# Performance work log

Hardware: AMD Instinct MI355X
Metric: run time of the kernel (lower is better)

The kernel has to match this reference:

```python
import math
import jax, jax.numpy as jnp
import numpy as np


def _bilinear_maps_sample(kv_feats, shapes_wh, start_ids, locs, map_ids):
    """Bilinear sampling from concatenated multi-level 2D maps.

    kv_feats: [BH, S, C] flattened (row-major, per level) feature maps
    shapes_wh: [L, 2] int (W, H) per level
    start_ids: [L] int start offset of each level in S
    locs: [BH, M, 2] normalized (x, y) in [0, 1]
    map_ids: [BH, M] int level index per sample
    returns [BH, M, C]
    """
    wh = shapes_wh[map_ids]                      # [BH, M, 2]
    W = wh[..., 0]
    H = wh[..., 1]
    start = start_ids[map_ids]                   # [BH, M]
    Wf = W.astype(locs.dtype)
    Hf = H.astype(locs.dtype)
    x = locs[..., 0] * Wf - 0.5                  # align_corners=False convention
    y = locs[..., 1] * Hf - 0.5
    x0 = jnp.floor(x)
    y0 = jnp.floor(y)
    out = jnp.zeros(locs.shape[:-1] + (kv_feats.shape[-1],), kv_feats.dtype)
    for dx in (0, 1):
        for dy in (0, 1):
            xi = x0 + dx
            yi = y0 + dy
            w = (1.0 - jnp.abs(x - xi)) * (1.0 - jnp.abs(y - yi))
            valid = (xi >= 0) & (xi < Wf) & (yi >= 0) & (yi < Hf)
            xi_c = jnp.clip(xi, 0, Wf - 1).astype(jnp.int32)
            yi_c = jnp.clip(yi, 0, Hf - 1).astype(jnp.int32)
            idx = start + yi_c * W + xi_c        # [BH, M]
            f = jnp.take_along_axis(kv_feats, idx[..., None], axis=1)
            out = out + jnp.where(valid, w, 0.0)[..., None] * f
    return out


def setup_inputs() -> dict:
    key = jax.random.key(0)
    ks = jax.random.split(key, 10)
    B, N, L, Hh, P = 2, 2048, 5, 8, 4
    in_size, sample_size = 256, 256
    qk_size, value_size = 256, 256
    kv_size = qk_size + value_size

    shapes = np.array([[128, 128], [64, 64], [32, 32], [16, 16], [8, 8]], np.int32)  # (H, W)
    flat = (shapes[:, 0] * shapes[:, 1]).astype(np.int64)
    start = np.concatenate([[0], np.cumsum(flat)[:-1]]).astype(np.int32)
    S = int(flat.sum())  # 21824

    # sampling_offsets bias: canonical Deformable-DETR grid init
    thetas = np.arange(Hh, dtype=np.float32) * (2.0 * math.pi / Hh)
    grid = np.stack([np.cos(thetas), np.sin(thetas)], axis=1)
    grid = grid / np.abs(grid).max(axis=1, keepdims=True)
    grid = np.tile(grid.reshape(Hh, 1, 1, 2), (1, L, 1, 1))
    sizes = np.arange(1, P + 1, dtype=np.float32).reshape(1, 1, P, 1)
    b_off = (sizes * grid).reshape(-1)           # [H*L*P*2]

    def lin(k, out_d, in_d):
        return jax.random.normal(k, (out_d, in_d), jnp.float32) * (1.0 / math.sqrt(in_d))

    return {
        "in_feats": jax.random.normal(ks[0], (B, N, in_size), jnp.float32),
        "sample_priors": jax.random.uniform(ks[1], (B, N, L, 2), jnp.float32),
        "sample_feats": jax.random.normal(ks[2], (B, S, sample_size), jnp.float32),
        "sample_map_shapes": jnp.asarray(shapes),
        "sample_map_start_ids": jnp.asarray(start),
        "W_off": jax.random.normal(ks[3], (Hh * L * P * 2, in_size), jnp.float32) * 0.02,
        "b_off": jnp.asarray(b_off),
        "W_q": lin(ks[4], qk_size, in_size),
        "b_q": jnp.zeros((qk_size,), jnp.float32),
        "W_kv": lin(ks[5], kv_size, sample_size),
        "b_kv": jnp.zeros((kv_size,), jnp.float32),
        "point_encs": jax.random.normal(ks[6], (Hh, L * P, qk_size // Hh), jnp.float32) * 0.02,
        "W_out": lin(ks[7], in_size, value_size),
        "b_out": jnp.zeros((in_size,), jnp.float32),
    }


def reference(in_feats, sample_priors, sample_feats, sample_map_shapes,
              sample_map_start_ids, W_off, b_off, W_q, b_q, W_kv, b_kv,
              point_encs, W_out, b_out):
    B, N = in_feats.shape[:2]
    Hh, LP, dqk = point_encs.shape
    L = sample_map_shapes.shape[0]
    P = LP // L

    # sampling offsets + locations (priors last dim == 2 path)
    off = (in_feats @ W_off.T + b_off).reshape(B, N, Hh, L, P, 2)
    shapes_wh = sample_map_shapes[:, ::-1]                      # fliplr -> (W, H)
    norm = shapes_wh.astype(in_feats.dtype)[None, None, None, :, None, :]
    locs = sample_priors[:, :, None, :, None, :] + off / norm    # [B,N,H,L,P,2]

    q = (in_feats @ W_q.T + b_q).reshape(B, N, Hh, dqk)
    kv = sample_feats @ W_kv.T + b_kv                            # [B,S,kv_size]
    ck = kv.shape[-1] // Hh
    kv = kv.reshape(B, -1, Hh, ck).transpose(0, 2, 1, 3).reshape(B * Hh, -1, ck)

    locs = locs.transpose(0, 2, 1, 3, 4, 5).reshape(B * Hh, N * L * P, 2)
    map_ids = jnp.broadcast_to(jnp.arange(L, dtype=jnp.int32)[None, None, :, None],
                               (B * Hh, N, L, P)).reshape(B * Hh, -1)

    sampled = _bilinear_maps_sample(kv, shapes_wh, sample_map_start_ids, locs, map_ids)
    sampled = sampled.reshape(B, Hh, N, LP, ck).transpose(0, 2, 1, 3, 4)  # [B,N,H,LP,ck]

    keys = sampled[..., :dqk] + point_encs                       # [B,N,H,LP,dqk]
    vals = sampled[..., dqk:]                                    # [B,N,H,LP,cv]
    attn = jax.nn.softmax(
        jnp.einsum('bnhd,bnhpd->bnhp', q / math.sqrt(dqk), keys), axis=-1)
    weighted = jnp.einsum('bnhp,bnhpd->bnhd', attn, vals).reshape(B, N, -1)
    return weighted @ W_out.T + b_out
```

## Files before the change

### kernel.cpp

```cpp
#include <hip/hip_runtime.h>
#include <cstddef>

#define B_  2
#define N_  2048
#define L_  5
#define HH  8
#define P_  4
#define S_  21824
#define DQK 32

using bf16x8 = __attribute__((ext_vector_type(8))) short;
using f32x4  = __attribute__((ext_vector_type(4))) float;
using us8    = __attribute__((ext_vector_type(8))) unsigned short;

__device__ __forceinline__ unsigned short f2b(float f) {
  unsigned u = __builtin_bit_cast(unsigned, f);
  u += 0x7FFFu + ((u >> 16) & 1u);
  return (unsigned short)(u >> 16);
}
__device__ __forceinline__ float b2f(unsigned short h) {
  return __builtin_bit_cast(float, ((unsigned)h) << 16);
}

__device__ __forceinline__ void gld_lds16(const void* g, void* l) {
  __builtin_amdgcn_global_load_lds(
      (const __attribute__((address_space(1))) unsigned int*)g,
      (__attribute__((address_space(3))) unsigned int*)l, 16, 0, 0);
}

template <int CTRL>
__device__ __forceinline__ float dppadd(float v) {
  const int x = __builtin_bit_cast(int, v);
  return v + __builtin_bit_cast(float,
      __builtin_amdgcn_update_dpp(x, x, CTRL, 0xF, 0xF, false));
}

#define E0 1396736
#define E1 1527808
#define E2 1658880
#define E3 1675264
#define E4 1683456
#define E5 1691648
#define E6 1703936
#define E7 1716224

__device__ __forceinline__ void cvt8_plain(const float* s, unsigned short* d, int u) {
  const float4 a = ((const float4*)s)[2 * u];
  const float4 b = ((const float4*)s)[2 * u + 1];
  us8 o;
  o[0] = f2b(a.x); o[1] = f2b(a.y); o[2] = f2b(a.z); o[3] = f2b(a.w);
  o[4] = f2b(b.x); o[5] = f2b(b.y); o[6] = f2b(b.z); o[7] = f2b(b.w);
  ((us8*)d)[u] = o;
}
__device__ __forceinline__ unsigned short f2b_lo(float x) {
  return f2b(x - b2f(f2b(x)));
}
__device__ __forceinline__ void cvt8_lo(const float* s, unsigned short* d, int u) {
  const float4 a = ((const float4*)s)[2 * u];
  const float4 b = ((const float4*)s)[2 * u + 1];
  us8 o;
  o[0] = f2b_lo(a.x); o[1] = f2b_lo(a.y); o[2] = f2b_lo(a.z); o[3] = f2b_lo(a.w);
  o[4] = f2b_lo(b.x); o[5] = f2b_lo(b.y); o[6] = f2b_lo(b.z); o[7] = f2b_lo(b.w);
  ((us8*)d)[u] = o;
}

__global__ __launch_bounds__(256) void cvt_all(
    const float* __restrict__ sfeats, const float* __restrict__ in_feats,
    const float* __restrict__ W_kv, const float* __restrict__ W_q,
    const float* __restrict__ W_out, const float* __restrict__ W_off,
    unsigned short* __restrict__ sf_bf, unsigned short* __restrict__ if_hi,
    unsigned short* __restrict__ if_lo, unsigned short* __restrict__ wkv_bf,
    unsigned short* __restrict__ wq_bf, unsigned short* __restrict__ wout_bf,
    unsigned short* __restrict__ woff_hi, unsigned short* __restrict__ woff_lo) {
  const int i = blockIdx.x * 256 + threadIdx.x;
  if      (i < E0) cvt8_plain(sfeats, sf_bf, i);
  else if (i < E1) cvt8_plain(in_feats, if_hi, i - E0);
  else if (i < E2) cvt8_lo(in_feats, if_lo, i - E1);
  else if (i < E3) cvt8_plain(W_kv, wkv_bf, i - E2);
  else if (i < E4) cvt8_plain(W_q, wq_bf, i - E3);
  else if (i < E5) cvt8_plain(W_out, wout_bf, i - E4);
  else if (i < E6) {
    const int u = i - E5;
    if ((u >> 5) < 320) cvt8_plain(W_off, woff_hi, u);
    else ((us8*)woff_hi)[u] = (us8)0;
  } else {
    const int u = i - E6;
    if ((u >> 5) < 320) cvt8_lo(W_off, woff_lo, u);
    else ((us8*)woff_lo)[u] = (us8)0;
  }
}

__device__ __forceinline__ void mfma_tile_k256(
    const unsigned short* __restrict__ Ap, const unsigned short* __restrict__ Wp,
    unsigned short* As, unsigned short* Bs,
    int row0, int col0, int wv, int wr, int wc, int fr, int fq,
    int srow, int sch, f32x4 (&acc)[4][4]) {
  for (int k0 = 0; k0 < 256; k0 += 64) {
#pragma unroll
    for (int i = 0; i < 4; ++i) {
      const int r = i * 32 + srow;
      const int ca = sch ^ (r & 7);
      gld_lds16(Ap + (size_t)(row0 + r) * 256 + k0 + ca * 8,
                As + (size_t)(i * 32 + wv * 8) * 64);
      gld_lds16(Wp + (size_t)(col0 + r) * 256 + k0 + ca * 8,
                Bs + (size_t)(i * 32 + wv * 8) * 64);
    }
    __syncthreads();
#pragma unroll
    for (int kk = 0; kk < 2; ++kk) {
      bf16x8 af[4], bfv[4];
#pragma unroll
      for (int i = 0; i < 4; ++i) {
        const int ar = wr * 64 + i * 16 + fr;
        const int cha = (kk * 4 + fq) ^ (ar & 7);
        af[i] = *(const bf16x8*)(As + ar * 64 + cha * 8);
        const int br = wc * 64 + i * 16 + fr;
        const int chb = (kk * 4 + fq) ^ (br & 7);
        bfv[i] = *(const bf16x8*)(Bs + br * 64 + chb * 8);
      }
#pragma unroll
      for (int i = 0; i < 4; ++i)
#pragma unroll
        for (int j = 0; j < 4; ++j)
          acc[i][j] = __builtin_amdgcn_mfma_f32_16x16x32_bf16(
              af[i], bfv[j], acc[i][j], 0, 0, 0);
    }
    __syncthreads();
  }
}

__global__ __launch_bounds__(256) void ubergemm(
    const unsigned short* __restrict__ sf_bf,
    const unsigned short* __restrict__ wkv_bf,
    const unsigned short* __restrict__ if_hi,
    const unsigned short* __restrict__ if_lo,
    const unsigned short* __restrict__ woff_hi,
    const unsigned short* __restrict__ woff_lo,
    const unsigned short* __restrict__ wq_bf,
    const float* __restrict__ b_kv, const float* __restrict__ b_off,
    const float* __restrict__ b_q,
    unsigned short* __restrict__ kvt, float* __restrict__ offb,
    float* __restrict__ qb) {
  __shared__ __align__(16) unsigned short As[128 * 64];
  __shared__ __align__(16) unsigned short Bs[128 * 64];

  const int tid = threadIdx.x;
  const int lane = tid & 63;
  const int wv = tid >> 6;
  const int wr = wv >> 1, wc = wv & 1;
  const int fr = lane & 15, fq = lane >> 4;
  const int srow = tid >> 3;
  const int sch = tid & 7;
  const int bx = blockIdx.x;

  int mode, nseg, row0, col0, ldc = 0, nbias = 0;
  const unsigned short *A0, *W0, *A1 = nullptr, *W1 = nullptr,
                       *A2 = nullptr, *W2 = nullptr;
  const float* bias;
  float* Cf = nullptr;
  if (bx < 1364) {
    mode = 1; nseg = 1; A0 = sf_bf; W0 = wkv_bf; bias = b_kv;
    col0 = (bx & 3) * 128; row0 = (bx >> 2) * 128;
  } else if (bx < 1460) {
    const int t = bx - 1364;
    mode = 0; nseg = 3;
    A0 = if_hi; W0 = woff_hi; A1 = if_hi; W1 = woff_lo; A2 = if_lo; W2 = woff_hi;
    bias = b_off; Cf = offb; ldc = 384; nbias = 320;
    col0 = (t % 3) * 128; row0 = (t / 3) * 128;
  } else {
    const int t = bx - 1460;
    mode = 0; nseg = 1; A0 = if_hi; W0 = wq_bf; bias = b_q;
    Cf = qb; ldc = 256; nbias = 256;
    col0 = (t & 1) * 128; row0 = (t >> 1) * 128;
  }

  f32x4 acc[4][4] = {};
  for (int s = 0; s < nseg; ++s) {
    const unsigned short* Ap = (s == 0) ? A0 : (s == 1) ? A1 : A2;
    const unsigned short* Wp = (s == 0) ? W0 : (s == 1) ? W1 : W2;
    mfma_tile_k256(Ap, Wp, As, Bs, row0, col0, wv, wr, wc, fr, fq, srow, sch, acc);
  }

#pragma unroll
  for (int j = 0; j < 4; ++j) {
    const int n = col0 + wc * 64 + j * 16 + fr;
    const float bv = (mode == 1) ? bias[n] : ((n < nbias) ? bias[n] : 0.f);
#pragma unroll
    for (int i = 0; i < 4; ++i) {
      const int mbase = row0 + wr * 64 + i * 16 + fq * 4;
#pragma unroll
      for (int r = 0; r < 4; ++r) {
        const int m = mbase + r;
        if (mode == 1) {
          const int b = (m >= S_) ? 1 : 0;
          const int s = m - b * S_;
          const int h = n >> 6, c = n & 63;
          kvt[((size_t)(b * HH + h) * S_ + s) * 64 + c] = f2b(acc[i][j][r] + bv);
        } else {
          Cf[(size_t)m * ldc + n] = acc[i][j][r] + bv;
        }
      }
    }
  }
}

__global__ __launch_bounds__(256) void gemm_out(
    const unsigned short* __restrict__ A, const unsigned short* __restrict__ Wt,
    const float* __restrict__ bias, float* __restrict__ C) {
  __shared__ __align__(16) unsigned short As[128 * 64];
  __shared__ __align__(16) unsigned short Bs[128 * 64];
  const int tid = threadIdx.x;
  const int lane = tid & 63;
  const int wv = tid >> 6;
  const int wr = wv >> 1, wc = wv & 1;
  const int fr = lane & 15, fq = lane >> 4;
  const int row0 = blockIdx.y * 128, col0 = blockIdx.x * 128;
  const int srow = tid >> 3, sch = tid & 7;
  f32x4 acc[4][4] = {};
  mfma_tile_k256(A, Wt, As, Bs, row0, col0, wv, wr, wc, fr, fq, srow, sch, acc);
#pragma unroll
  for (int j = 0; j < 4; ++j) {
    const int n = col0 + wc * 64 + j * 16 + fr;
    const float bv = bias[n];
#pragma unroll
    for (int i = 0; i < 4; ++i) {
      const int mbase = row0 + wr * 64 + i * 16 + fq * 4;
#pragma unroll
      for (int r = 0; r < 4; ++r)
        C[(size_t)(mbase + r) * 256 + n] = acc[i][j][r] + bv;
    }
  }
}

__global__ __launch_bounds__(256) void sample_attn4(
    const unsigned short* __restrict__ kvt,
    const float* __restrict__ offb,
    const float* __restrict__ qb,
    const float* __restrict__ priors,
    const int* __restrict__ shapes,
    const int* __restrict__ starts,
    const float* __restrict__ pencs,
    unsigned short* __restrict__ wtd) {
  __shared__ __align__(16) int pbuf[4][20][8];
  const int wv = threadIdx.x >> 6;
  const int lane = threadIdx.x & 63;
  const int beta = blockIdx.x;
  const int sig = (beta & 7) * 2 + ((beta >> 3) & 1);
  const int chunk = beta >> 4;
  const int h = sig & 7;
  const int b = sig >> 3;
  const int bn = b * N_ + chunk * 4 + wv;
  const int j = lane & 31;
  const int half = lane >> 5;

  if (lane < 20) {
    const int pp = lane;
    const int l = pp >> 2;
    const float2 oxy = *(const float2*)(offb + (size_t)bn * 384 + h * 40 + pp * 2);
    const float2 pxy = *(const float2*)(priors + ((size_t)bn * 5 + l) * 2);
    const int Wd = shapes[l * 2 + 1];
    const int Hd = shapes[l * 2 + 0];
    const int st = starts[l];
    const float Wf = (float)Wd, Hf = (float)Hd;
    const float x = (pxy.x + oxy.x / Wf) * Wf - 0.5f;
    const float y = (pxy.y + oxy.y / Hf) * Hf - 0.5f;
    const float x0f = floorf(x), y0f = floorf(y);
    const float fx = x - x0f, fy = y - y0f;
    const int xi = (int)x0f, yi = (int)y0f;
    int a[4]; float w[4];
#pragma unroll
    for (int dy = 0; dy < 2; ++dy)
#pragma unroll
      for (int dx = 0; dx < 2; ++dx) {
        const int xc = xi + dx, yc = yi + dy;
        const bool valid = (xc >= 0) & (xc < Wd) & (yc >= 0) & (yc < Hd);
        const float wt = (dx ? fx : 1.f - fx) * (dy ? fy : 1.f - fy);
        const int xcc = min(max(xc, 0), Wd - 1);
        const int ycc = min(max(yc, 0), Hd - 1);
        a[dy * 2 + dx] = (st + ycc * Wd + xcc) * 32;
        w[dy * 2 + dx] = valid ? wt : 0.f;
      }
    *(int4*)&pbuf[wv][pp][0] = make_int4(a[0], a[1], a[2], a[3]);
    *(float4*)&pbuf[wv][pp][4] = make_float4(w[0], w[1], w[2], w[3]);
  }

  const int jc = j & 15;
  float2 q2 = *(const float2*)(qb + (size_t)bn * 256 + h * DQK + 2 * jc);
  q2.x *= 0.17677669529663687f;
  q2.y *= 0.17677669529663687f;
  float qpe[10];
#pragma unroll
  for (int i = 0; i < 10; ++i) {
    const float2 pe = *(const float2*)(
        pencs + ((size_t)h * 20 + 2 * i + half) * DQK + 2 * jc);
    qpe[i] = q2.x * pe.x + q2.y * pe.y;
  }

  const unsigned* kvd = (const unsigned*)(kvt + (size_t)(b * HH + h) * (S_ * 64));
  int4 aa[2]; float4 ww[2]; unsigned g[2][4];
  aa[0] = *(const int4*)&pbuf[wv][half][0];
  ww[0] = *(const float4*)&pbuf[wv][half][4];
  g[0][0] = kvd[(unsigned)aa[0].x + j];
  g[0][1] = kvd[(unsigned)aa[0].y + j];
  g[0][2] = kvd[(unsigned)aa[0].z + j];
  g[0][3] = kvd[(unsigned)aa[0].w + j];

  float2 sam[10];
  float lg[10];
#pragma unroll
  for (int i = 0; i < 10; ++i) {
    const int cur = i & 1, nxt = cur ^ 1;
    if (i < 9) {
      aa[nxt] = *(const int4*)&pbuf[wv][2 * (i + 1) + half][0];
      ww[nxt] = *(const float4*)&pbuf[wv][2 * (i + 1) + half][4];
      g[nxt][0] = kvd[(unsigned)aa[nxt].x + j];
      g[nxt][1] = kvd[(unsigned)aa[nxt].y + j];
      g[nxt][2] = kvd[(unsigned)aa[nxt].z + j];
      g[nxt][3] = kvd[(unsigned)aa[nxt].w + j];
    }
    const float4 wt = ww[cur];
    const unsigned g0 = g[cur][0], g1 = g[cur][1], g2 = g[cur][2], g3 = g[cur][3];
    const float lo0 = __builtin_bit_cast(float, g0 << 16);
    const float hi0 = __builtin_bit_cast(float, g0 & 0xFFFF0000u);
    const float lo1 = __builtin_bit_cast(float, g1 << 16);
    const float hi1 = __builtin_bit_cast(float, g1 & 0xFFFF0000u);
    const float lo2 = __builtin_bit_cast(float, g2 << 16);
    const float hi2 = __builtin_bit_cast(float, g2 & 0xFFFF0000u);
    const float lo3 = __builtin_bit_cast(float, g3 << 16);
    const float hi3 = __builtin_bit_cast(float, g3 & 0xFFFF0000u);
    float vx = wt.x * lo0;  vx = fmaf(wt.y, lo1, vx);
    vx = fmaf(wt.z, lo2, vx); vx = fmaf(wt.w, lo3, vx);
    float vy = wt.x * hi0;  vy = fmaf(wt.y, hi1, vy);
    vy = fmaf(wt.z, hi2, vy); vy = fmaf(wt.w, hi3, vy);
    sam[i].x = vx; sam[i].y = vy;
    float part = (j < 16) ? fmaf(q2.x, vx, fmaf(q2.y, vy, qpe[i])) : 0.f;
    part = dppadd<0xB1>(part);
    part = dppadd<0x4E>(part);
    part = dppadd<0x124>(part);
    part = dppadd<0x128>(part);
    lg[i] = part + __shfl_xor(part, 16, 64);
  }

  float mx = lg[0];
#pragma unroll
  for (int i = 1; i < 10; ++i) mx = fmaxf(mx, lg[i]);
  mx = fmaxf(mx, __shfl_xor(mx, 32, 64));
  float se = 0.f;
#pragma unroll
  for (int i = 0; i < 10; ++i) {
    lg[i] = __expf(lg[i] - mx);
    se += lg[i];
  }
  se += __shfl_xor(se, 32, 64);
  const float inv = 1.f / se;

  float ax = 0.f, ay = 0.f;
#pragma unroll
  for (int i = 0; i < 10; ++i) {
    ax = fmaf(lg[i], sam[i].x, ax);
    ay = fmaf(lg[i], sam[i].y, ay);
  }
  ax += __shfl_xor(ax, 32, 64);
  ay += __shfl_xor(ay, 32, 64);

  if (half == 0 && j >= 16) {
    const unsigned u = (unsigned)f2b(ax * inv) | ((unsigned)f2b(ay * inv) << 16);
    ((unsigned*)wtd)[(size_t)bn * 128 + h * 16 + (j - 16)] = u;
  }
}

extern "C" void kernel_launch(void* const* d_in, const int* in_sizes, int n_in,
                              void* d_out, int out_size, void* d_ws, size_t ws_size,
                              hipStream_t stream) {
  const float* in_feats = (const float*)d_in[0];
  const float* priors   = (const float*)d_in[1];
  const float* sfeats   = (const float*)d_in[2];
  const int*   shapes   = (const int*)d_in[3];
  const int*   starts   = (const int*)d_in[4];
  const float* W_off    = (const float*)d_in[5];
  const float* b_off    = (const float*)d_in[6];
  const float* W_q      = (const float*)d_in[7];
  const float* b_q      = (const float*)d_in[8];
  const float* W_kv     = (const float*)d_in[9];
  const float* b_kv     = (const float*)d_in[10];
  const float* pencs    = (const float*)d_in[11];
  const float* W_out    = (const float*)d_in[12];
  const float* b_out    = (const float*)d_in[13];
  float* out = (float*)d_out;

  char* w = (char*)d_ws;
  unsigned short* kvt = (unsigned short*)w;
  w += (size_t)B_ * HH * S_ * 64 * 2;
  unsigned short* sf_bf = (unsigned short*)w;
  w += (size_t)B_ * S_ * 256 * 2;
  unsigned short* if_hi = (unsigned short*)w; w += (size_t)4096 * 256 * 2;
  unsigned short* if_lo = (unsigned short*)w; w += (size_t)4096 * 256 * 2;
  unsigned short* wkv_bf = (unsigned short*)w;  w += (size_t)512 * 256 * 2;
  unsigned short* wq_bf  = (unsigned short*)w;  w += (size_t)256 * 256 * 2;
  unsigned short* wout_bf = (unsigned short*)w; w += (size_t)256 * 256 * 2;
  unsigned short* woff_hi = (unsigned short*)w; w += (size_t)384 * 256 * 2;
  unsigned short* woff_lo = (unsigned short*)w; w += (size_t)384 * 256 * 2;
  float* offb = (float*)w;  w += (size_t)4096 * 384 * 4;
  float* qb   = (float*)w;  w += (size_t)4096 * 256 * 4;
  unsigned short* wtd_bf = (unsigned short*)w; w += (size_t)4096 * 256 * 2;

  cvt_all<<<E7 / 256, 256, 0, stream>>>(
      sfeats, in_feats, W_kv, W_q, W_out, W_off,
      sf_bf, if_hi, if_lo, wkv_bf, wq_bf, wout_bf, woff_hi, woff_lo);

  ubergemm<<<1524, 256, 0, stream>>>(
      sf_bf, wkv_bf, if_hi, if_lo, woff_hi, woff_lo, wq_bf,
      b_kv, b_off, b_q, kvt, offb, qb);

  sample_attn4<<<(B_ * N_ * HH) / 4, 256, 0, stream>>>(
      kvt, offb, qb, priors, shapes, starts, pencs, wtd_bf);

  gemm_out<<<dim3(2, 32), 256, 0, stream>>>(wtd_bf, wout_bf, b_out, out);
}
```

Baseline: 99.91 us.

## Fuse sample_feats bf16 conversion into KV GEMM A-tile load

The KV projection GEMM now reads fp32 sample features directly, converting them to bf16 with packed-convert instructions while staging into LDS. This removes the separate conversion pass, which wrote and then re-read a bf16 copy of the largest input. The small offset/query GEMM blocks are moved to the front, and KV tiles are reordered in groups of 8 rows per column for L2 reuse of the A rows. The in_feats hi/lo split is also merged into one pass. The A-tile load is no longer an asynchronous global-to-LDS copy, so it now goes through registers.

```diff
diff --git a/kernel.cpp b/kernel.cpp
--- a/kernel.cpp
+++ b/kernel.cpp
@@ -21,6 +21,11 @@
 __device__ __forceinline__ float b2f(unsigned short h) {
   return __builtin_bit_cast(float, ((unsigned)h) << 16);
 }
+__device__ __forceinline__ unsigned cvtpk(float lo, float hi) {
+  unsigned r;
+  asm("v_cvt_pk_bf16_f32 %0, %1, %2" : "=v"(r) : "v"(lo), "v"(hi));
+  return r;
+}
 
 __device__ __forceinline__ void gld_lds16(const void* g, void* l) {
   __builtin_amdgcn_global_load_lds(
@@ -35,14 +40,12 @@
       __builtin_amdgcn_update_dpp(x, x, CTRL, 0xF, 0xF, false));
 }
 
-#define E0 1396736
-#define E1 1527808
-#define E2 1658880
-#define E3 1675264
-#define E4 1683456
-#define E5 1691648
-#define E6 1703936
-#define E7 1716224
+#define F0 131072
+#define F1 147456
+#define F2 155648
+#define F3 163840
+#define F4 176128
+#define F5 188416
 
 __device__ __forceinline__ void cvt8_plain(const float* s, unsigned short* d, int u) {
   const float4 a = ((const float4*)s)[2 * u];
@@ -63,34 +66,71 @@
   o[4] = f2b_lo(b.x); o[5] = f2b_lo(b.y); o[6] = f2b_lo(b.z); o[7] = f2b_lo(b.w);
   ((us8*)d)[u] = o;
 }
+__device__ __forceinline__ void cvt8_both(const float* s, unsigned short* dh,
+                                          unsigned short* dl, int u) {
+  const float4 a = ((const float4*)s)[2 * u];
+  const float4 b = ((const float4*)s)[2 * u + 1];
+  us8 oh, ol;
+  const float v[8] = {a.x, a.y, a.z, a.w, b.x, b.y, b.z, b.w};
+#pragma unroll
+  for (int k = 0; k < 8; ++k) {
+    const unsigned short h = f2b(v[k]);
+    oh[k] = h;
+    ol[k] = f2b(v[k] - b2f(h));
+  }
+  ((us8*)dh)[u] = oh;
+  ((us8*)dl)[u] = ol;
+}
 
 __global__ __launch_bounds__(256) void cvt_all(
-    const float* __restrict__ sfeats, const float* __restrict__ in_feats,
-    const float* __restrict__ W_kv, const float* __restrict__ W_q,
-    const float* __restrict__ W_out, const float* __restrict__ W_off,
-    unsigned short* __restrict__ sf_bf, unsigned short* __restrict__ if_hi,
-    unsigned short* __restrict__ if_lo, unsigned short* __restrict__ wkv_bf,
-    unsigned short* __restrict__ wq_bf, unsigned short* __restrict__ wout_bf,
-    unsigned short* __restrict__ woff_hi, unsigned short* __restrict__ woff_lo) {
+    const float* __restrict__ in_feats, const float* __restrict__ W_kv,
+    const float* __restrict__ W_q, const float* __restrict__ W_out,
+    const float* __restrict__ W_off,
+    unsigned short* __restrict__ if_hi, unsigned short* __restrict__ if_lo,
+    unsigned short* __restrict__ wkv_bf, unsigned short* __restrict__ wq_bf,
+    unsigned short* __restrict__ wout_bf, unsigned short* __restrict__ woff_hi,
+    unsigned short* __restrict__ woff_lo) {
   const int i = blockIdx.x * 256 + threadIdx.x;
-  if      (i < E0) cvt8_plain(sfeats, sf_bf, i);
-  else if (i < E1) cvt8_plain(in_feats, if_hi, i - E0);
-  else if (i < E2) cvt8_lo(in_feats, if_lo, i - E1);
-  else if (i < E3) cvt8_plain(W_kv, wkv_bf, i - E2);
-  else if (i < E4) cvt8_plain(W_q, wq_bf, i - E3);
-  else if (i < E5) cvt8_plain(W_out, wout_bf, i - E4);
-  else if (i < E6) {
-    const int u = i - E5;
+  if      (i < F0) cvt8_both(in_feats, if_hi, if_lo, i);
+  else if (i < F1) cvt8_plain(W_kv, wkv_bf, i - F0);
+  else if (i < F2) cvt8_plain(W_q, wq_bf, i - F1);
+  else if (i < F3) cvt8_plain(W_out, wout_bf, i - F2);
+  else if (i < F4) {
+    const int u = i - F3;
     if ((u >> 5) < 320) cvt8_plain(W_off, woff_hi, u);
     else ((us8*)woff_hi)[u] = (us8)0;
   } else {
-    const int u = i - E6;
+    const int u = i - F4;
     if ((u >> 5) < 320) cvt8_lo(W_off, woff_lo, u);
     else ((us8*)woff_lo)[u] = (us8)0;
   }
 }
 
-__device__ __forceinline__ void mfma_tile_k256(
+__device__ __forceinline__ void mfma_compute(
+    const unsigned short* As, const unsigned short* Bs,
+    int wr, int wc, int fr, int fq, f32x4 (&acc)[4][4]) {
+#pragma unroll
+  for (int kk = 0; kk < 2; ++kk) {
+    bf16x8 af[4], bfv[4];
+#pragma unroll
+    for (int i = 0; i < 4; ++i) {
+      const int ar = wr * 64 + i * 16 + fr;
+      const int cha = (kk * 4 + fq) ^ (ar & 7);
+      af[i] = *(const bf16x8*)(As + ar * 64 + cha * 8);
+      const int br = wc * 64 + i * 16 + fr;
+      const int chb = (kk * 4 + fq) ^ (br & 7);
+      bfv[i] = *(const bf16x8*)(Bs + br * 64 + chb * 8);
+    }
+#pragma unroll
+    for (int i = 0; i < 4; ++i)
+#pragma unroll
+      for (int j = 0; j < 4; ++j)
+        acc[i][j] = __builtin_amdgcn_mfma_f32_16x16x32_bf16(
+            af[i], bfv[j], acc[i][j], 0, 0, 0);
+  }
+}
+
+__device__ __forceinline__ void mfma_tile_bf16(
     const unsigned short* __restrict__ Ap, const unsigned short* __restrict__ Wp,
     unsigned short* As, unsigned short* Bs,
     int row0, int col0, int wv, int wr, int wc, int fr, int fq,
@@ -106,31 +146,47 @@
                 Bs + (size_t)(i * 32 + wv * 8) * 64);
     }
     __syncthreads();
-#pragma unroll
-    for (int kk = 0; kk < 2; ++kk) {
-      bf16x8 af[4], bfv[4];
-#pragma unroll
-      for (int i = 0; i < 4; ++i) {
-        const int ar = wr * 64 + i * 16 + fr;
-        const int cha = (kk * 4 + fq) ^ (ar & 7);
-        af[i] = *(const bf16x8*)(As + ar * 64 + cha * 8);
-        const int br = wc * 64 + i * 16 + fr;
-        const int chb = (kk * 4 + fq) ^ (br & 7);
-        bfv[i] = *(const bf16x8*)(Bs + br * 64 + chb * 8);
-      }
-#pragma unroll
-      for (int i = 0; i < 4; ++i)
-#pragma unroll
-        for (int j = 0; j < 4; ++j)
-          acc[i][j] = __builtin_amdgcn_mfma_f32_16x16x32_bf16(
-              af[i], bfv[j], acc[i][j], 0, 0, 0);
-    }
+    mfma_compute(As, Bs, wr, wc, fr, fq, acc);
     __syncthreads();
   }
 }
 
+__device__ __forceinline__ void mfma_tile_f32A(
+    const float* __restrict__ Af, const unsigned short* __restrict__ Wp,
+    unsigned short* As, unsigned short* Bs,
+    int row0, int col0, int wv, int wr, int wc, int fr, int fq,
+    int srow, int sch, int tid, f32x4 (&acc)[4][4]) {
+  const int arow = tid >> 1;
+  const int cb = (tid & 1) * 4;
+  for (int k0 = 0; k0 < 256; k0 += 64) {
+#pragma unroll
+    for (int i = 0; i < 4; ++i) {
+      const int r = i * 32 + srow;
+      const int ca = sch ^ (r & 7);
+      gld_lds16(Wp + (size_t)(col0 + r) * 256 + k0 + ca * 8,
+                Bs + (size_t)(i * 32 + wv * 8) * 64);
+    }
+    const float* arp = Af + (size_t)(row0 + arow) * 256 + k0;
+#pragma unroll
+    for (int c = 0; c < 4; ++c) {
+      const int ch = cb + c;
+      const float4 a0 = *(const float4*)(arp + ch * 8);
+      const float4 a1 = *(const float4*)(arp + ch * 8 + 4);
+      uint4 u;
+      u.x = cvtpk(a0.x, a0.y);
+      u.y = cvtpk(a0.z, a0.w);
+      u.z = cvtpk(a1.x, a1.y);
+      u.w = cvtpk(a1.z, a1.w);
+      *(uint4*)(As + arow * 64 + (ch ^ (arow & 7)) * 8) = u;
+    }
+    __syncthreads();
+    mfma_compute(As, Bs, wr, wc, fr, fq, acc);
+    __syncthreads();
+  }
+}
+
 __global__ __launch_bounds__(256) void ubergemm(
-    const unsigned short* __restrict__ sf_bf,
+    const float* __restrict__ sfeats,
     const unsigned short* __restrict__ wkv_bf,
     const unsigned short* __restrict__ if_hi,
     const unsigned short* __restrict__ if_lo,
@@ -153,45 +209,51 @@
   const int sch = tid & 7;
   const int bx = blockIdx.x;
 
-  int mode, nseg, row0, col0, ldc = 0, nbias = 0;
-  const unsigned short *A0, *W0, *A1 = nullptr, *W1 = nullptr,
-                       *A2 = nullptr, *W2 = nullptr;
+  f32x4 acc[4][4] = {};
+  int kvmode = 0, row0, col0, ldc = 0, nbias = 0;
   const float* bias;
   float* Cf = nullptr;
-  if (bx < 1364) {
-    mode = 1; nseg = 1; A0 = sf_bf; W0 = wkv_bf; bias = b_kv;
-    col0 = (bx & 3) * 128; row0 = (bx >> 2) * 128;
-  } else if (bx < 1460) {
-    const int t = bx - 1364;
-    mode = 0; nseg = 3;
-    A0 = if_hi; W0 = woff_hi; A1 = if_hi; W1 = woff_lo; A2 = if_lo; W2 = woff_hi;
+
+  if (bx < 96) {
+    col0 = (bx % 3) * 128; row0 = (bx / 3) * 128;
     bias = b_off; Cf = offb; ldc = 384; nbias = 320;
-    col0 = (t % 3) * 128; row0 = (t / 3) * 128;
+    mfma_tile_bf16(if_hi, woff_hi, As, Bs, row0, col0, wv, wr, wc, fr, fq, srow, sch, acc);
+    mfma_tile_bf16(if_hi, woff_lo, As, Bs, row0, col0, wv, wr, wc, fr, fq, srow, sch, acc);
+    mfma_tile_bf16(if_lo, woff_hi, As, Bs, row0, col0, wv, wr, wc, fr, fq, srow, sch, acc);
+  } else if (bx < 160) {
+    const int t = bx - 96;
+    col0 = (t & 1) * 128; row0 = (t >> 1) * 128;
+    bias = b_q; Cf = qb; ldc = 256; nbias = 256;
+    mfma_tile_bf16(if_hi, wq_bf, As, Bs, row0, col0, wv, wr, wc, fr, fq, srow, sch, acc);
   } else {
-    const int t = bx - 1460;
-    mode = 0; nseg = 1; A0 = if_hi; W0 = wq_bf; bias = b_q;
-    Cf = qb; ldc = 256; nbias = 256;
-    col0 = (t & 1) * 128; row0 = (t >> 1) * 128;
-  }
-
-  f32x4 acc[4][4] = {};
-  for (int s = 0; s < nseg; ++s) {
-    const unsigned short* Ap = (s == 0) ? A0 : (s == 1) ? A1 : A2;
-    const unsigned short* Wp = (s == 0) ? W0 : (s == 1) ? W1 : W2;
-    mfma_tile_k256(Ap, Wp, As, Bs, row0, col0, wv, wr, wc, fr, fq, srow, sch, acc);
+    const int t = bx - 160;
+    int row, col;
+    if (t < 1344) {
+      const int x = t & 7;
+      const int s2 = t >> 3;
+      col = s2 & 3;
+      row = (s2 >> 2) * 8 + x;
+    } else {
+      const int u2 = t - 1344;
+      row = 336 + (u2 >> 2);
+      col = u2 & 3;
+    }
+    row0 = row * 128; col0 = col * 128;
+    kvmode = 1; bias = b_kv;
+    mfma_tile_f32A(sfeats, wkv_bf, As, Bs, row0, col0, wv, wr, wc, fr, fq, srow, sch, tid, acc);
   }
 
 #pragma unroll
   for (int j = 0; j < 4; ++j) {
     const int n = col0 + wc * 64 + j * 16 + fr;
-    const float bv = (mode == 1) ? bias[n] : ((n < nbias) ? bias[n] : 0.f);
+    const float bv = kvmode ? bias[n] : ((n < nbias) ? bias[n] : 0.f);
 #pragma unroll
     for (int i = 0; i < 4; ++i) {
       const int mbase = row0 + wr * 64 + i * 16 + fq * 4;
 #pragma unroll
       for (int r = 0; r < 4; ++r) {
         const int m = mbase + r;
-        if (mode == 1) {
+        if (kvmode) {
           const int b = (m >= S_) ? 1 : 0;
           const int s = m - b * S_;
           const int h = n >> 6, c = n & 63;
@@ -217,7 +279,7 @@
   const int row0 = blockIdx.y * 128, col0 = blockIdx.x * 128;
   const int srow = tid >> 3, sch = tid & 7;
   f32x4 acc[4][4] = {};
-  mfma_tile_k256(A, Wt, As, Bs, row0, col0, wv, wr, wc, fr, fq, srow, sch, acc);
+  mfma_tile_bf16(A, Wt, As, Bs, row0, col0, wv, wr, wc, fr, fq, srow, sch, acc);
 #pragma unroll
   for (int j = 0; j < 4; ++j) {
     const int n = col0 + wc * 64 + j * 16 + fr;
@@ -391,8 +453,6 @@
   char* w = (char*)d_ws;
   unsigned short* kvt = (unsigned short*)w;
   w += (size_t)B_ * HH * S_ * 64 * 2;
-  unsigned short* sf_bf = (unsigned short*)w;
-  w += (size_t)B_ * S_ * 256 * 2;
   unsigned short* if_hi = (unsigned short*)w; w += (size_t)4096 * 256 * 2;
   unsigned short* if_lo = (unsigned short*)w; w += (size_t)4096 * 256 * 2;
   unsigned short* wkv_bf = (unsigned short*)w;  w += (size_t)512 * 256 * 2;
@@ -404,12 +464,12 @@
   float* qb   = (float*)w;  w += (size_t)4096 * 256 * 4;
   unsigned short* wtd_bf = (unsigned short*)w; w += (size_t)4096 * 256 * 2;
 
-  cvt_all<<<E7 / 256, 256, 0, stream>>>(
-      sfeats, in_feats, W_kv, W_q, W_out, W_off,
-      sf_bf, if_hi, if_lo, wkv_bf, wq_bf, wout_bf, woff_hi, woff_lo);
+  cvt_all<<<F5 / 256, 256, 0, stream>>>(
+      in_feats, W_kv, W_q, W_out, W_off,
+      if_hi, if_lo, wkv_bf, wq_bf, wout_bf, woff_hi, woff_lo);
 
   ubergemm<<<1524, 256, 0, stream>>>(
-      sf_bf, wkv_bf, if_hi, if_lo, woff_hi, woff_lo, wq_bf,
+      sfeats, wkv_bf, if_hi, if_lo, woff_hi, woff_lo, wq_bf,
       b_kv, b_off, b_q, kvt, offb, qb);
 
   sample_attn4<<<(B_ * N_ * HH) / 4, 256, 0, stream>>>(
```

New measurement: 101.6 us. Within noise of the previous version (+1.7%).

## Double-buffer KV GEMM, swap operands for packed bf16 stores, reorder blocks

Applied to the files above, without the earlier changes.

The KV projection path in the fused GEMM kernel now runs a double-buffered pipeline with K-steps of 32. Each next stage's global-to-LDS load is issued before the current stage's MFMAs, with explicit vmcnt waits and raw barriers. MFMA operands are swapped so each lane holds 4 consecutive output columns, which lets the epilogue write packed bf16 pairs with v_cvt_pk_bf16_f32 instead of scalar stores. The small offset and q GEMM blocks are moved to the front, and KV blocks are remapped in groups of 8 for L2 locality. This adds padded grid blocks that exit early, plus more hand-written synchronisation to get right.

```diff
diff --git a/kernel.cpp b/kernel.cpp
--- a/kernel.cpp
+++ b/kernel.cpp
@@ -20,6 +20,11 @@
 }
 __device__ __forceinline__ float b2f(unsigned short h) {
   return __builtin_bit_cast(float, ((unsigned)h) << 16);
+}
+__device__ __forceinline__ unsigned cvtpk(float lo, float hi) {
+  unsigned r;
+  asm("v_cvt_pk_bf16_f32 %0, %1, %2" : "=v"(r) : "v"(lo), "v"(hi));
+  return r;
 }
 
 __device__ __forceinline__ void gld_lds16(const void* g, void* l) {
@@ -90,7 +95,31 @@
   }
 }
 
-__device__ __forceinline__ void mfma_tile_k256(
+__device__ __forceinline__ void mfma_compute(
+    const unsigned short* As, const unsigned short* Bs,
+    int wr, int wc, int fr, int fq, f32x4 (&acc)[4][4]) {
+#pragma unroll
+  for (int kk = 0; kk < 2; ++kk) {
+    bf16x8 af[4], bfv[4];
+#pragma unroll
+    for (int i = 0; i < 4; ++i) {
+      const int ar = wr * 64 + i * 16 + fr;
+      const int cha = (kk * 4 + fq) ^ (ar & 7);
+      af[i] = *(const bf16x8*)(As + ar * 64 + cha * 8);
+      const int br = wc * 64 + i * 16 + fr;
+      const int chb = (kk * 4 + fq) ^ (br & 7);
+      bfv[i] = *(const bf16x8*)(Bs + br * 64 + chb * 8);
+    }
+#pragma unroll
+    for (int i = 0; i < 4; ++i)
+#pragma unroll
+      for (int j = 0; j < 4; ++j)
+        acc[i][j] = __builtin_amdgcn_mfma_f32_16x16x32_bf16(
+            af[i], bfv[j], acc[i][j], 0, 0, 0);
+  }
+}
+
+__device__ __forceinline__ void mfma_tile_bf16(
     const unsigned short* __restrict__ Ap, const unsigned short* __restrict__ Wp,
     unsigned short* As, unsigned short* Bs,
     int row0, int col0, int wv, int wr, int wc, int fr, int fq,
@@ -106,25 +135,7 @@
                 Bs + (size_t)(i * 32 + wv * 8) * 64);
     }
     __syncthreads();
-#pragma unroll
-    for (int kk = 0; kk < 2; ++kk) {
-      bf16x8 af[4], bfv[4];
-#pragma unroll
-      for (int i = 0; i < 4; ++i) {
-        const int ar = wr * 64 + i * 16 + fr;
-        const int cha = (kk * 4 + fq) ^ (ar & 7);
-        af[i] = *(const bf16x8*)(As + ar * 64 + cha * 8);
-        const int br = wc * 64 + i * 16 + fr;
-        const int chb = (kk * 4 + fq) ^ (br & 7);
-        bfv[i] = *(const bf16x8*)(Bs + br * 64 + chb * 8);
-      }
-#pragma unroll
-      for (int i = 0; i < 4; ++i)
-#pragma unroll
-        for (int j = 0; j < 4; ++j)
-          acc[i][j] = __builtin_amdgcn_mfma_f32_16x16x32_bf16(
-              af[i], bfv[j], acc[i][j], 0, 0, 0);
-    }
+    mfma_compute(As, Bs, wr, wc, fr, fq, acc);
     __syncthreads();
   }
 }
@@ -141,65 +152,127 @@
     const float* __restrict__ b_q,
     unsigned short* __restrict__ kvt, float* __restrict__ offb,
     float* __restrict__ qb) {
-  __shared__ __align__(16) unsigned short As[128 * 64];
-  __shared__ __align__(16) unsigned short Bs[128 * 64];
+  __shared__ __align__(16) unsigned short lds[128 * 128];
 
   const int tid = threadIdx.x;
   const int lane = tid & 63;
   const int wv = tid >> 6;
   const int wr = wv >> 1, wc = wv & 1;
   const int fr = lane & 15, fq = lane >> 4;
+  const int bx = blockIdx.x;
+
+  f32x4 acc[4][4] = {};
+
+  if (bx >= 160) {
+    const int t = bx - 160;
+    const int x = t & 7;
+    const int idx = t >> 3;
+    const int c = idx & 3;
+    const int g = (idx >> 2) * 8 + x;
+    if (g >= 341) return;
+    const int row0 = g * 128;
+    const int col0 = c * 128;
+
+    unsigned short* Ab[2] = {lds, lds + 4096};
+    unsigned short* Bb[2] = {lds + 8192, lds + 12288};
+
+#define KV_STAGE(KK, BUF)                                                     \
+    {                                                                         \
+      _Pragma("unroll")                                                       \
+      for (int ld = 0; ld < 2; ++ld) {                                        \
+        const int ci = ld * 256 + tid;                                        \
+        const int rw = ci >> 2, cc = ci & 3;                                  \
+        const int ca = cc ^ (rw & 3);                                         \
+        gld_lds16(sf_bf + (size_t)(row0 + rw) * 256 + (KK) * 32 + ca * 8,     \
+                  Ab[BUF] + (size_t)(ld * 256 + wv * 64) * 8);                \
+        gld_lds16(wkv_bf + (size_t)(col0 + rw) * 256 + (KK) * 32 + ca * 8,    \
+                  Bb[BUF] + (size_t)(ld * 256 + wv * 64) * 8);                \
+      }                                                                       \
+    }
+
+    KV_STAGE(0, 0);
+#pragma unroll
+    for (int k = 0; k < 8; ++k) {
+      if (k < 7) {
+        KV_STAGE(k + 1, (k + 1) & 1);
+        asm volatile("s_waitcnt vmcnt(4)" ::: "memory");
+      } else {
+        asm volatile("s_waitcnt vmcnt(0)" ::: "memory");
+      }
+      __builtin_amdgcn_s_barrier();
+      __builtin_amdgcn_sched_barrier(0);
+      const unsigned short* Ac = Ab[k & 1];
+      const unsigned short* Bc = Bb[k & 1];
+      bf16x8 af[4], bfv[4];
+#pragma unroll
+      for (int i = 0; i < 4; ++i) {
+        const int ar = wr * 64 + i * 16 + fr;
+        af[i] = *(const bf16x8*)(Ac + (ar * 4 + (fq ^ (ar & 3))) * 8);
+      }
+#pragma unroll
+      for (int j = 0; j < 4; ++j) {
+        const int nr = wc * 64 + j * 16 + fr;
+        bfv[j] = *(const bf16x8*)(Bc + (nr * 4 + (fq ^ (nr & 3))) * 8);
+      }
+#pragma unroll
+      for (int j = 0; j < 4; ++j)
+#pragma unroll
+        for (int i = 0; i < 4; ++i)
+          acc[j][i] = __builtin_amdgcn_mfma_f32_16x16x32_bf16(
+              bfv[j], af[i], acc[j][i], 0, 0, 0);
+      __builtin_amdgcn_s_barrier();
+    }
+#undef KV_STAGE
+
+#pragma unroll
+    for (int j = 0; j < 4; ++j) {
+      const int c0 = col0 + wc * 64 + j * 16 + fq * 4;
+      const float4 bb = *(const float4*)(b_kv + c0);
+      const int h = c0 >> 6;
+      const int cc = c0 & 63;
+#pragma unroll
+      for (int i = 0; i < 4; ++i) {
+        const int sl = row0 + wr * 64 + i * 16 + fr;
+        const int b = (sl >= S_) ? 1 : 0;
+        const int s = sl - b * S_;
+        unsigned* dst = (unsigned*)(kvt + ((size_t)(b * HH + h) * S_ + s) * 64 + cc);
+        dst[0] = cvtpk(acc[j][i][0] + bb.x, acc[j][i][1] + bb.y);
+        dst[1] = cvtpk(acc[j][i][2] + bb.z, acc[j][i][3] + bb.w);
+      }
+    }
+    return;
+  }
+
+  unsigned short* As = lds;
+  unsigned short* Bs = lds + 128 * 64;
   const int srow = tid >> 3;
   const int sch = tid & 7;
-  const int bx = blockIdx.x;
-
-  int mode, nseg, row0, col0, ldc = 0, nbias = 0;
-  const unsigned short *A0, *W0, *A1 = nullptr, *W1 = nullptr,
-                       *A2 = nullptr, *W2 = nullptr;
+  int row0, col0, ldc, nbias;
   const float* bias;
-  float* Cf = nullptr;
-  if (bx < 1364) {
-    mode = 1; nseg = 1; A0 = sf_bf; W0 = wkv_bf; bias = b_kv;
-    col0 = (bx & 3) * 128; row0 = (bx >> 2) * 128;
-  } else if (bx < 1460) {
-    const int t = bx - 1364;
-    mode = 0; nseg = 3;
-    A0 = if_hi; W0 = woff_hi; A1 = if_hi; W1 = woff_lo; A2 = if_lo; W2 = woff_hi;
+  float* Cf;
+  if (bx < 96) {
+    col0 = (bx % 3) * 128; row0 = (bx / 3) * 128;
     bias = b_off; Cf = offb; ldc = 384; nbias = 320;
-    col0 = (t % 3) * 128; row0 = (t / 3) * 128;
+    mfma_tile_bf16(if_hi, woff_hi, As, Bs, row0, col0, wv, wr, wc, fr, fq, srow, sch, acc);
+    mfma_tile_bf16(if_hi, woff_lo, As, Bs, row0, col0, wv, wr, wc, fr, fq, srow, sch, acc);
+    mfma_tile_bf16(if_lo, woff_hi, As, Bs, row0, col0, wv, wr, wc, fr, fq, srow, sch, acc);
   } else {
-    const int t = bx - 1460;
-    mode = 0; nseg = 1; A0 = if_hi; W0 = wq_bf; bias = b_q;
-    Cf = qb; ldc = 256; nbias = 256;
+    const int t = bx - 96;
     col0 = (t & 1) * 128; row0 = (t >> 1) * 128;
-  }
-
-  f32x4 acc[4][4] = {};
-  for (int s = 0; s < nseg; ++s) {
-    const unsigned short* Ap = (s == 0) ? A0 : (s == 1) ? A1 : A2;
-    const unsigned short* Wp = (s == 0) ? W0 : (s == 1) ? W1 : W2;
-    mfma_tile_k256(Ap, Wp, As, Bs, row0, col0, wv, wr, wc, fr, fq, srow, sch, acc);
+    bias = b_q; Cf = qb; ldc = 256; nbias = 256;
+    mfma_tile_bf16(if_hi, wq_bf, As, Bs, row0, col0, wv, wr, wc, fr, fq, srow, sch, acc);
   }
 
 #pragma unroll
   for (int j = 0; j < 4; ++j) {
     const int n = col0 + wc * 64 + j * 16 + fr;
-    const float bv = (mode == 1) ? bias[n] : ((n < nbias) ? bias[n] : 0.f);
+    const float bv = (n < nbias) ? bias[n] : 0.f;
 #pragma unroll
     for (int i = 0; i < 4; ++i) {
       const int mbase = row0 + wr * 64 + i * 16 + fq * 4;
 #pragma unroll
-      for (int r = 0; r < 4; ++r) {
-        const int m = mbase + r;
-        if (mode == 1) {
-          const int b = (m >= S_) ? 1 : 0;
-          const int s = m - b * S_;
-          const int h = n >> 6, c = n & 63;
-          kvt[((size_t)(b * HH + h) * S_ + s) * 64 + c] = f2b(acc[i][j][r] + bv);
-        } else {
-          Cf[(size_t)m * ldc + n] = acc[i][j][r] + bv;
-        }
-      }
+      for (int r = 0; r < 4; ++r)
+        Cf[(size_t)(mbase + r) * ldc + n] = acc[i][j][r] + bv;
     }
   }
 }
@@ -217,7 +290,7 @@
   const int row0 = blockIdx.y * 128, col0 = blockIdx.x * 128;
   const int srow = tid >> 3, sch = tid & 7;
   f32x4 acc[4][4] = {};
-  mfma_tile_k256(A, Wt, As, Bs, row0, col0, wv, wr, wc, fr, fq, srow, sch, acc);
+  mfma_tile_bf16(A, Wt, As, Bs, row0, col0, wv, wr, wc, fr, fq, srow, sch, acc);
 #pragma unroll
   for (int j = 0; j < 4; ++j) {
     const int n = col0 + wc * 64 + j * 16 + fr;
@@ -408,7 +481,7 @@
       sfeats, in_feats, W_kv, W_q, W_out, W_off,
       sf_bf, if_hi, if_lo, wkv_bf, wq_bf, wout_bf, woff_hi, woff_lo);
 
-  ubergemm<<<1524, 256, 0, stream>>>(
+  ubergemm<<<1536, 256, 0, stream>>>(
       sf_bf, wkv_bf, if_hi, if_lo, woff_hi, woff_lo, wq_bf,
       b_kv, b_off, b_q, kvt, offb, qb);
 
```

New measurement: 87.09 us. 1.15x faster.
